# Optimization experiments

Measured on AMD Instinct MI355X. Metric: run time of the kernel, lower is better.

Reference implementation:

```python
import jax, jax.numpy as jnp
import numpy as np

NUM_SPLITS = 64
UNITS_PER_SPLIT = 64
IN_DIM = 4096          # divisible by NUM_SPLITS -> 64 input features per split
OUT_DIM = NUM_SPLITS * UNITS_PER_SPLIT  # 4096
BATCH = 4096
BN_EPS = 1e-3          # keras BatchNormalization default epsilon


def make_mask():
    # block_diag of NUM_SPLITS ones-blocks of shape (IN_DIM//NUM_SPLITS, UNITS_PER_SPLIT)
    din_per = IN_DIM // NUM_SPLITS
    return jnp.kron(jnp.eye(NUM_SPLITS, dtype=jnp.float32),
                    jnp.ones((din_per, UNITS_PER_SPLIT), dtype=jnp.float32))


def setup_inputs() -> dict:
    key = jax.random.key(0)
    k_x, k_w = jax.random.split(key)
    x = jax.random.normal(k_x, (BATCH, IN_DIM), dtype=jnp.float32)
    weight = jax.random.normal(k_w, (IN_DIM, OUT_DIM), dtype=jnp.float32) * (2.0 / IN_DIM) ** 0.5
    bias = jnp.full((OUT_DIM,), 0.1, dtype=jnp.float32)
    gamma = jnp.ones((OUT_DIM,), dtype=jnp.float32)
    beta = jnp.zeros((OUT_DIM,), dtype=jnp.float32)
    return {"x": x, "weight": weight, "bias": bias, "gamma": gamma, "beta": beta}


def reference(x, weight, bias, gamma, beta):
    mask = make_mask()  # [IN_DIM, OUT_DIM] block-diagonal 0/1
    # masked dense: only block-diagonal entries of weight participate
    out = jnp.matmul(x, weight * mask) + bias  # [B, OUT_DIM]
    # BatchNorm, training=True: batch statistics (biased variance), keras eps=1e-3
    mean = jnp.mean(out, axis=0)
    var = jnp.mean(jnp.square(out - mean), axis=0)
    out = (out - mean) * jax.lax.rsqrt(var + BN_EPS) * gamma + beta
    return jax.nn.relu(out)
```

## Files before the change

kernel.cpp:

```cpp
#include <hip/hip_runtime.h>
#include <hip/hip_bf16.h>

#define BATCH 4096
#define DIM 4096
#define NSPLIT 64
#define ROWS_PB 128
#define BN_EPS 1e-3f

typedef __attribute__((ext_vector_type(8))) short bf16x8;
typedef __attribute__((ext_vector_type(4))) float f32x4;

__device__ inline unsigned short f2bf(float f) {
    union { float f; unsigned int u; } c; c.f = f;
    unsigned int u = c.u;
    u += 0x7FFFu + ((u >> 16) & 1u);
    return (unsigned short)(u >> 16);
}

__global__ __launch_bounds__(256) void gemm_stats(
    const float* __restrict__ x, const float* __restrict__ w,
    const float* __restrict__ bias,
    unsigned short* __restrict__ wsout,
    float* __restrict__ gsum, float* __restrict__ gsumsq)
{
    __shared__ unsigned short xs[ROWS_PB][72];
    __shared__ unsigned short wt[64][72];
    __shared__ float bcol[64];
    __shared__ float csum[64], csumsq[64];

    const int s  = blockIdx.y;
    const int r0 = blockIdx.x * ROWS_PB;
    const int t  = threadIdx.x;

    if (t < 64) { bcol[t] = bias[s*64 + t]; csum[t] = 0.f; csumsq[t] = 0.f; }

    for (int i = t; i < ROWS_PB * 16; i += 256) {
        int row = i >> 4, c4 = i & 15;
        float4 v = *(const float4*)(x + (size_t)(r0 + row) * DIM + s*64 + c4*4);
        ushort4 u;
        u.x = f2bf(v.x); u.y = f2bf(v.y); u.z = f2bf(v.z); u.w = f2bf(v.w);
        *(ushort4*)&xs[row][c4 * 4] = u;
    }
    for (int i = t; i < 64 * 64; i += 256) {
        int k = i >> 6, n = i & 63;
        wt[n][k] = f2bf(w[(size_t)(s*64 + k) * DIM + s*64 + n]);
    }
    __syncthreads();

    const int lane = t & 63;
    const int wave = t >> 6;
    const int quad = lane >> 4;
    const int l16  = lane & 15;
    const int wrow = wave * 32;

    f32x4 acc[2][4];
    for (int rt = 0; rt < 2; rt++)
        for (int ct = 0; ct < 4; ct++) {
            float b = bcol[ct*16 + l16];
            acc[rt][ct] = (f32x4){b, b, b, b};
        }

    bf16x8 afrag[2][2], bfrag[4][2];
    for (int rt = 0; rt < 2; rt++)
        for (int kk = 0; kk < 2; kk++)
            afrag[rt][kk] = *(const bf16x8*)&xs[wrow + rt*16 + l16][kk*32 + quad*8];
    for (int ct = 0; ct < 4; ct++)
        for (int kk = 0; kk < 2; kk++)
            bfrag[ct][kk] = *(const bf16x8*)&wt[ct*16 + l16][kk*32 + quad*8];

    for (int kk = 0; kk < 2; kk++)
        for (int rt = 0; rt < 2; rt++)
            for (int ct = 0; ct < 4; ct++)
                acc[rt][ct] = __builtin_amdgcn_mfma_f32_16x16x32_bf16(
                    afrag[rt][kk], bfrag[ct][kk], acc[rt][ct], 0, 0, 0);

    float s1[4], s2[4];
    for (int ct = 0; ct < 4; ct++) { s1[ct] = 0.f; s2[ct] = 0.f; }
    for (int rt = 0; rt < 2; rt++)
        for (int ct = 0; ct < 4; ct++) {
            int col = ct*16 + l16;
            for (int r = 0; r < 4; r++) {
                float v = acc[rt][ct][r];
                int row = r0 + wrow + rt*16 + quad*4 + r;
                wsout[(size_t)row * DIM + s*64 + col] = f2bf(v);
                s1[ct] += v; s2[ct] += v * v;
            }
        }
    for (int ct = 0; ct < 4; ct++) {
        float a = s1[ct], b = s2[ct];
        a += __shfl_xor(a, 16); b += __shfl_xor(b, 16);
        a += __shfl_xor(a, 32); b += __shfl_xor(b, 32);
        if (quad == 0) {
            atomicAdd(&csum[ct*16 + l16], a);
            atomicAdd(&csumsq[ct*16 + l16], b);
        }
    }
    __syncthreads();
    if (t < 64) {
        atomicAdd(&gsum[s*64 + t], csum[t]);
        atomicAdd(&gsumsq[s*64 + t], csumsq[t]);
    }
}

__global__ __launch_bounds__(256) void finalize_stats(
    const float* __restrict__ gsum, const float* __restrict__ gsumsq,
    const float* __restrict__ gamma, const float* __restrict__ beta,
    float* __restrict__ scale, float* __restrict__ shiftv)
{
    int j = blockIdx.x * 256 + threadIdx.x;
    float mean = gsum[j] * (1.f / BATCH);
    float var  = gsumsq[j] * (1.f / BATCH) - mean * mean;
    float rstd = rsqrtf(var + BN_EPS);
    float sc = gamma[j] * rstd;
    scale[j]  = sc;
    shiftv[j] = beta[j] - mean * sc;
}

__global__ __launch_bounds__(256) void normalize(
    const unsigned short* __restrict__ wsout,
    const float* __restrict__ scale, const float* __restrict__ shiftv,
    float* __restrict__ out)
{
    size_t i = ((size_t)blockIdx.x * 256 + threadIdx.x) * 8;
    int col = (int)(i & (DIM - 1));
    uint4 u = *(const uint4*)(wsout + i);
    float4 sc0 = *(const float4*)(scale + col);
    float4 sc1 = *(const float4*)(scale + col + 4);
    float4 sh0 = *(const float4*)(shiftv + col);
    float4 sh1 = *(const float4*)(shiftv + col + 4);
    float v0 = __uint_as_float(u.x << 16), v1 = __uint_as_float(u.x & 0xFFFF0000u);
    float v2 = __uint_as_float(u.y << 16), v3 = __uint_as_float(u.y & 0xFFFF0000u);
    float v4 = __uint_as_float(u.z << 16), v5 = __uint_as_float(u.z & 0xFFFF0000u);
    float v6 = __uint_as_float(u.w << 16), v7 = __uint_as_float(u.w & 0xFFFF0000u);
    float4 o0, o1;
    o0.x = fmaxf(fmaf(v0, sc0.x, sh0.x), 0.f);
    o0.y = fmaxf(fmaf(v1, sc0.y, sh0.y), 0.f);
    o0.z = fmaxf(fmaf(v2, sc0.z, sh0.z), 0.f);
    o0.w = fmaxf(fmaf(v3, sc0.w, sh0.w), 0.f);
    o1.x = fmaxf(fmaf(v4, sc1.x, sh1.x), 0.f);
    o1.y = fmaxf(fmaf(v5, sc1.y, sh1.y), 0.f);
    o1.z = fmaxf(fmaf(v6, sc1.z, sh1.z), 0.f);
    o1.w = fmaxf(fmaf(v7, sc1.w, sh1.w), 0.f);
    *(float4*)(out + i)     = o0;
    *(float4*)(out + i + 4) = o1;
}

extern "C" void kernel_launch(void* const* d_in, const int* in_sizes, int n_in,
                              void* d_out, int out_size, void* d_ws, size_t ws_size,
                              hipStream_t stream) {
    const float* x     = (const float*)d_in[0];
    const float* w     = (const float*)d_in[1];
    const float* bias  = (const float*)d_in[2];
    const float* gamma = (const float*)d_in[3];
    const float* beta  = (const float*)d_in[4];
    float* out = (float*)d_out;

    unsigned short* wsout = (unsigned short*)d_ws;
    float* gsum   = (float*)((char*)d_ws + (size_t)BATCH * DIM * 2);
    float* gsumsq = gsum + DIM;
    float* scale  = gsum + 2 * DIM;
    float* shiftv = gsum + 3 * DIM;

    hipMemsetAsync(gsum, 0, 2 * DIM * sizeof(float), stream);

    gemm_stats<<<dim3(BATCH / ROWS_PB, NSPLIT), 256, 0, stream>>>(
        x, w, bias, wsout, gsum, gsumsq);
    finalize_stats<<<DIM / 256, 256, 0, stream>>>(gsum, gsumsq, gamma, beta, scale, shiftv);
    normalize<<<(size_t)BATCH * DIM / 8 / 256, 256, 0, stream>>>(wsout, scale, shiftv, out);
}
```

Baseline: 187.3 us.

## Fuse GEMM, batch stats and normalize into one cooperative kernel with grid sync

Replaces the three-kernel pipeline (GEMM+stats, finalize, normalize) with a single cooperative kernel of 512 blocks. Each block keeps its 512x64 output tile in registers, writes per-block partial sums, waits at a grid-wide sync, computes scale and shift, then writes the final ReLU output directly. This removes the bf16 intermediate round-trip through global memory, the memset and two extra launches, and replaces the global atomics with deterministic partial sums. The cost is heavy register pressure (128 accumulator floats per thread), reliance on a grid barrier, and a possible fallback to the old path if the cooperative launch fails.

Measured after the change: 242.5 us. 29.5% more time.

```diff
diff --git a/kernel.cpp b/kernel.cpp
--- a/kernel.cpp
+++ b/kernel.cpp
@@ -1,5 +1,8 @@
 #include <hip/hip_runtime.h>
 #include <hip/hip_bf16.h>
+#include <hip/hip_cooperative_groups.h>
+
+namespace cg = cooperative_groups;
 
 #define BATCH 4096
 #define DIM 4096
@@ -15,6 +18,150 @@
     unsigned int u = c.u;
     u += 0x7FFFu + ((u >> 16) & 1u);
     return (unsigned short)(u >> 16);
+}
+
+__global__ __launch_bounds__(256, 2) void fused(
+    const float* __restrict__ x, const float* __restrict__ w,
+    const float* __restrict__ bias, const float* __restrict__ gamma,
+    const float* __restrict__ beta, float* __restrict__ out,
+    float* __restrict__ part)
+{
+    __shared__ unsigned short wt[64][72];
+    __shared__ unsigned short xs[128][72];
+    __shared__ float bcol[64];
+    __shared__ float red_s1[4][64], red_s2[4][64];
+    __shared__ float scol[64], shcol[64];
+
+    const int bx  = blockIdx.x;
+    const int s   = bx >> 3;
+    const int cgp = bx & 7;
+    const int t   = threadIdx.x;
+    const int lane = t & 63, wave = t >> 6;
+    const int quad = lane >> 4, l16 = lane & 15;
+
+    for (int i = t; i < 1024; i += 256) {
+        int k = i >> 4, c4 = i & 15;
+        float4 v = *(const float4*)(w + (size_t)(s*64 + k) * DIM + s*64 + c4*4);
+        wt[c4*4 + 0][k] = f2bf(v.x);
+        wt[c4*4 + 1][k] = f2bf(v.y);
+        wt[c4*4 + 2][k] = f2bf(v.z);
+        wt[c4*4 + 3][k] = f2bf(v.w);
+    }
+    if (t < 64) bcol[t] = bias[s*64 + t];
+    __syncthreads();
+
+    bf16x8 bfrag[4][2];
+    #pragma unroll
+    for (int ct = 0; ct < 4; ct++)
+        #pragma unroll
+        for (int kk = 0; kk < 2; kk++)
+            bfrag[ct][kk] = *(const bf16x8*)&wt[ct*16 + l16][kk*32 + quad*8];
+
+    f32x4 acc[4][2][4];
+    float s1[4], s2[4];
+    #pragma unroll
+    for (int ct = 0; ct < 4; ct++) { s1[ct] = 0.f; s2[ct] = 0.f; }
+
+    for (int j = 0; j < 4; j++) {
+        int r0 = (cgp*4 + j) * ROWS_PB;
+        #pragma unroll
+        for (int it = 0; it < 8; it++) {
+            int i = t + it * 256;
+            int row = i >> 4, c4 = i & 15;
+            float4 v = *(const float4*)(x + (size_t)(r0 + row) * DIM + s*64 + c4*4);
+            ushort4 u;
+            u.x = f2bf(v.x); u.y = f2bf(v.y); u.z = f2bf(v.z); u.w = f2bf(v.w);
+            *(ushort4*)&xs[row][c4*4] = u;
+        }
+        __syncthreads();
+
+        #pragma unroll
+        for (int rt = 0; rt < 2; rt++)
+            #pragma unroll
+            for (int ct = 0; ct < 4; ct++) {
+                float b = bcol[ct*16 + l16];
+                acc[j][rt][ct] = (f32x4){b, b, b, b};
+            }
+
+        bf16x8 af[2][2];
+        #pragma unroll
+        for (int rt = 0; rt < 2; rt++)
+            #pragma unroll
+            for (int kk = 0; kk < 2; kk++)
+                af[rt][kk] = *(const bf16x8*)&xs[wave*32 + rt*16 + l16][kk*32 + quad*8];
+
+        #pragma unroll
+        for (int kk = 0; kk < 2; kk++)
+            #pragma unroll
+            for (int rt = 0; rt < 2; rt++)
+                #pragma unroll
+                for (int ct = 0; ct < 4; ct++)
+                    acc[j][rt][ct] = __builtin_amdgcn_mfma_f32_16x16x32_bf16(
+                        af[rt][kk], bfrag[ct][kk], acc[j][rt][ct], 0, 0, 0);
+
+        #pragma unroll
+        for (int rt = 0; rt < 2; rt++)
+            #pragma unroll
+            for (int ct = 0; ct < 4; ct++)
+                #pragma unroll
+                for (int r = 0; r < 4; r++) {
+                    float v = acc[j][rt][ct][r];
+                    s1[ct] += v; s2[ct] += v * v;
+                }
+        __syncthreads();
+    }
+
+    #pragma unroll
+    for (int ct = 0; ct < 4; ct++) {
+        float a = s1[ct], b = s2[ct];
+        a += __shfl_xor(a, 16); b += __shfl_xor(b, 16);
+        a += __shfl_xor(a, 32); b += __shfl_xor(b, 32);
+        if (quad == 0) {
+            red_s1[wave][ct*16 + l16] = a;
+            red_s2[wave][ct*16 + l16] = b;
+        }
+    }
+    __syncthreads();
+    if (t < 64) {
+        float a = red_s1[0][t] + red_s1[1][t] + red_s1[2][t] + red_s1[3][t];
+        float b = red_s2[0][t] + red_s2[1][t] + red_s2[2][t] + red_s2[3][t];
+        part[(size_t)bx * 128 + t]      = a;
+        part[(size_t)bx * 128 + 64 + t] = b;
+    }
+
+    cg::this_grid().sync();
+
+    if (t < 64) {
+        float a = 0.f, b = 0.f;
+        #pragma unroll
+        for (int i = 0; i < 8; i++) {
+            a += part[(size_t)(s*8 + i) * 128 + t];
+            b += part[(size_t)(s*8 + i) * 128 + 64 + t];
+        }
+        float mean = a * (1.f / BATCH);
+        float var  = b * (1.f / BATCH) - mean * mean;
+        float rstd = rsqrtf(var + BN_EPS);
+        float sc = gamma[s*64 + t] * rstd;
+        scol[t]  = sc;
+        shcol[t] = beta[s*64 + t] - mean * sc;
+    }
+    __syncthreads();
+
+    #pragma unroll
+    for (int j = 0; j < 4; j++)
+        #pragma unroll
+        for (int rt = 0; rt < 2; rt++)
+            #pragma unroll
+            for (int ct = 0; ct < 4; ct++) {
+                int col = ct*16 + l16;
+                float sc = scol[col], sh = shcol[col];
+                #pragma unroll
+                for (int r = 0; r < 4; r++) {
+                    float v = fmaxf(fmaf(acc[j][rt][ct][r], sc, sh), 0.f);
+                    int row = cgp*512 + j*128 + wave*32 + rt*16 + quad*4 + r;
+                    out[(size_t)row * DIM + s*64 + col] = v;
+                }
+            }
 }
 
 __global__ __launch_bounds__(256) void gemm_stats(
@@ -47,10 +194,8 @@
     }
     __syncthreads();
 
-    const int lane = t & 63;
-    const int wave = t >> 6;
-    const int quad = lane >> 4;
-    const int l16  = lane & 15;
+    const int lane = t & 63, wave = t >> 6;
+    const int quad = lane >> 4, l16 = lane & 15;
     const int wrow = wave * 32;
 
     f32x4 acc[2][4];
@@ -153,18 +298,25 @@
     const float* bias  = (const float*)d_in[2];
     const float* gamma = (const float*)d_in[3];
     const float* beta  = (const float*)d_in[4];
-    float* out = (float*)d_out;
-
-    unsigned short* wsout = (unsigned short*)d_ws;
-    float* gsum   = (float*)((char*)d_ws + (size_t)BATCH * DIM * 2);
-    float* gsumsq = gsum + DIM;
-    float* scale  = gsum + 2 * DIM;
-    float* shiftv = gsum + 3 * DIM;
-
-    hipMemsetAsync(gsum, 0, 2 * DIM * sizeof(float), stream);
-
-    gemm_stats<<<dim3(BATCH / ROWS_PB, NSPLIT), 256, 0, stream>>>(
-        x, w, bias, wsout, gsum, gsumsq);
-    finalize_stats<<<DIM / 256, 256, 0, stream>>>(gsum, gsumsq, gamma, beta, scale, shiftv);
-    normalize<<<(size_t)BATCH * DIM / 8 / 256, 256, 0, stream>>>(wsout, scale, shiftv, out);
-}
+    float* out  = (float*)d_out;
+    float* part = (float*)d_ws;
+
+    void* args[] = {(void*)&x, (void*)&w, (void*)&bias, (void*)&gamma,
+                    (void*)&beta, (void*)&out, (void*)&part};
+    hipError_t err = hipLaunchCooperativeKernel((void*)fused, dim3(512), dim3(256),
+                                                args, 0, stream);
+    if (err != hipSuccess) {
+        unsigned short* wsout = (unsigned short*)d_ws;
+        float* gsum   = (float*)((char*)d_ws + (size_t)BATCH * DIM * 2);
+        float* gsumsq = gsum + DIM;
+        float* scale  = gsum + 2 * DIM;
+        float* shiftv = gsum + 3 * DIM;
+        hipMemsetAsync(gsum, 0, 2 * DIM * sizeof(float), stream);
+        gemm_stats<<<dim3(BATCH / ROWS_PB, NSPLIT), 256, 0, stream>>>(
+            x, w, bias, wsout, gsum, gsumsq);
+        finalize_stats<<<DIM / 256, 256, 0, stream>>>(gsum, gsumsq, gamma, beta,
+                                                      scale, shiftv);
+        normalize<<<(size_t)BATCH * DIM / 8 / 256, 256, 0, stream>>>(
+            wsout, scale, shiftv, out);
+    }
+}
```
